# Kernel optimization log

Measured on AMD Instinct MI355X. Metric: run time of the kernel, lower is better.

## Reference

```python
import jax, jax.numpy as jnp
import numpy as np


def setup_inputs() -> dict:
    key = jax.random.key(0)
    kx, kw = jax.random.split(key)
    B, C, H, W, K = 16, 256, 128, 128, 7
    x = jax.random.normal(kx, (B, C, H, W), dtype=jnp.float32)
    # module initializes w with uniform(-0.1, 0.1)
    w = jax.random.uniform(kw, (C, K, K), dtype=jnp.float32, minval=-0.1, maxval=0.1)
    return {"x": x, "w": w}


def reference(x, w):
    # PolarConv2D forward intent: unfold(2,K,S).unfold(3,K,S) then per-channel
    # contraction of each (K,K) patch with w[c] -> depthwise convolution.
    # out[b,c,i,j] = sum_{k1,k2} x[b,c,i*S+k1, j*S+k2] * w[c,k1,k2]
    # Implemented as a grouped conv (feature_group_count=C) so the K*K-times
    # redundant unfolded tensor is never materialized.
    C = w.shape[0]
    kern = w[:, None, :, :]  # OIHW with I=1 (depthwise)
    out = jax.lax.conv_general_dilated(
        x, kern,
        window_strides=(1, 1),
        padding="VALID",
        dimension_numbers=("NCHW", "OIHW", "NCHW"),
        feature_group_count=C,
    )
    return out  # (B, C, H-K+1, W-K+1)
```

## Files before the change

### kernel.cpp

```cpp
#include <hip/hip_runtime.h>


#define BATCH 16
#define CHAN  256
#define H_IN  128
#define W_IN  128
#define KS    7
#define H_OUT 122
#define W_OUT 122

typedef float v2f __attribute__((ext_vector_type(2)));

__device__ __forceinline__ float sgpr_bcast(float v) {
    return __int_as_float(__builtin_amdgcn_readfirstlane(__float_as_int(v)));
}

__global__ __launch_bounds__(256)
void dwconv7x7_kernel(const float* __restrict__ x,
                      const float* __restrict__ w,
                      float* __restrict__ out) {
    const int lane = threadIdx.x & 63;
    const int img  = blockIdx.x;
    const int q    = threadIdx.x >> 6;
    const int ch   = img & (CHAN - 1);

    int c = 2 * lane;
    if (lane >= 32) c -= 6;
    const int r0 = 30 * q;

    const float* __restrict__ wp = w + ch * (KS * KS);
    float wr[KS * KS];
    #pragma unroll
    for (int i = 0; i < KS * KS; ++i) wr[i] = sgpr_bcast(wp[i]);

    const float* __restrict__ xq =
        x + (size_t)img * (H_IN * W_IN) + (size_t)r0 * W_IN + c;
    float* __restrict__ oq =
        out + (size_t)img * (H_OUT * W_OUT) + (size_t)r0 * W_OUT + c;

    float acc[KS][2] = {};
    float f[8];

    #define LOADW() do {                                                   \
        const v2f a0 = *reinterpret_cast<const v2f*>(xq);                  \
        const v2f a1 = *reinterpret_cast<const v2f*>(xq + 2);              \
        const v2f a2 = *reinterpret_cast<const v2f*>(xq + 4);              \
        const v2f a3 = *reinterpret_cast<const v2f*>(xq + 6);              \
        f[0] = a0.x; f[1] = a0.y; f[2] = a1.x; f[3] = a1.y;                \
        f[4] = a2.x; f[5] = a2.y; f[6] = a3.x; f[7] = a3.y; } while (0)

    #define ACCUM(SLOT, KY) do {                                           \
        _Pragma("unroll")                                                  \
        for (int kx = 0; kx < 7; ++kx) {                                   \
            const float wv = wr[(KY) * 7 + kx];                            \
            acc[(SLOT)][0] = fmaf(f[kx],     wv, acc[(SLOT)][0]);          \
            acc[(SLOT)][1] = fmaf(f[kx + 1], wv, acc[(SLOT)][1]);          \
        } } while (0)

    #define MAINSTEP(U) do {                                               \
        LOADW();                                                           \
        _Pragma("unroll")                                                  \
        for (int ky = 0; ky < KS; ++ky)                                    \
            ACCUM((6 + (U) - ky + 7) % KS, ky);                            \
        v2f v; v.x = acc[(U)][0]; v.y = acc[(U)][1];                       \
        __builtin_nontemporal_store(v, reinterpret_cast<v2f*>(oq));        \
        acc[(U)][0] = 0.f; acc[(U)][1] = 0.f;                              \
        xq += W_IN; oq += W_OUT; } while (0)

    #pragma unroll
    for (int s = 0; s < 6; ++s) {
        LOADW();
        #pragma unroll
        for (int ky = 0; ky <= s; ++ky)
            ACCUM((s - ky) % KS, ky);
        xq += W_IN;
    }

    for (int sb = 0; sb < 4; ++sb) {
        #pragma unroll
        for (int u = 0; u < 7; ++u) {
            MAINSTEP(u);
        }
    }

    #pragma unroll
    for (int t = 0; t < 4; ++t) {
        MAINSTEP(t);
    }

    #undef LOADW
    #undef ACCUM
    #undef MAINSTEP
}

extern "C" void kernel_launch(void* const* d_in, const int* in_sizes, int n_in,
                              void* d_out, int out_size, void* d_ws, size_t ws_size,
                              hipStream_t stream) {
    const float* x = (const float*)d_in[0];
    const float* w = (const float*)d_in[1];
    float* out = (float*)d_out;

    dim3 grid(BATCH * CHAN, 1, 1);
    dim3 block(256, 1, 1);
    dwconv7x7_kernel<<<grid, block, 0, stream>>>(x, w, out);
}
```

Baseline: 95.44 us.

## Stage input rows into LDS via async global_load_lds with multi-buffered pipeline

Instead of each lane loading overlapping 8-float windows straight from global memory, each wave asynchronously copies pairs of input rows into a 4-slot LDS ring buffer using global_load_lds. Manual vmcnt waits keep several row stages in flight while FMAs run. The accumulation is also reorganised into packed v2f FMAs over an 8-slot rotating accumulator. The hand-tuned waitcnt values and the LDS aliasing across stages carry correctness risk, and the removed compiler-visible memory dependencies could hide races because there is no barrier between LDS writes and reads.

```diff
diff --git a/kernel.cpp b/kernel.cpp
--- a/kernel.cpp
+++ b/kernel.cpp
@@ -1,4 +1,5 @@
 #include <hip/hip_runtime.h>
+#include <stdint.h>
 
 
 #define BATCH 16
@@ -19,9 +20,11 @@
 void dwconv7x7_kernel(const float* __restrict__ x,
                       const float* __restrict__ w,
                       float* __restrict__ out) {
+    __shared__ float lds[4][4][256];
+
     const int lane = threadIdx.x & 63;
+    const int q    = threadIdx.x >> 6;
     const int img  = blockIdx.x;
-    const int q    = threadIdx.x >> 6;
     const int ch   = img & (CHAN - 1);
 
     int c = 2 * lane;
@@ -33,64 +36,114 @@
     #pragma unroll
     for (int i = 0; i < KS * KS; ++i) wr[i] = sgpr_bcast(wp[i]);
 
-    const float* __restrict__ xq =
-        x + (size_t)img * (H_IN * W_IN) + (size_t)r0 * W_IN + c;
-    float* __restrict__ oq =
+    const float* xstage =
+        x + (size_t)img * (H_IN * W_IN) + (size_t)r0 * W_IN + lane * 4;
+    float* oq =
         out + (size_t)img * (H_OUT * W_OUT) + (size_t)r0 * W_OUT + c;
 
-    float acc[KS][2] = {};
-    float f[8];
+    v2f acc[8];
+    #pragma unroll
+    for (int i = 0; i < 8; ++i) { acc[i].x = 0.f; acc[i].y = 0.f; }
 
-    #define LOADW() do {                                                   \
-        const v2f a0 = *reinterpret_cast<const v2f*>(xq);                  \
-        const v2f a1 = *reinterpret_cast<const v2f*>(xq + 2);              \
-        const v2f a2 = *reinterpret_cast<const v2f*>(xq + 4);              \
-        const v2f a3 = *reinterpret_cast<const v2f*>(xq + 6);              \
-        f[0] = a0.x; f[1] = a0.y; f[2] = a1.x; f[3] = a1.y;                \
-        f[4] = a2.x; f[5] = a2.y; f[6] = a3.x; f[7] = a3.y; } while (0)
+    #define STAGE(SLOT) do {                                               \
+        asm volatile("" ::: "memory");                                     \
+        __builtin_amdgcn_global_load_lds(                                  \
+            (const __attribute__((address_space(1))) void*)xstage,         \
+            (__attribute__((address_space(3))) void*)&lds[q][SLOT][0],     \
+            16, 0, 0);                                                     \
+        xstage += 2 * W_IN; } while (0)
 
-    #define ACCUM(SLOT, KY) do {                                           \
+    #define WAITV(N) asm volatile("s_waitcnt vmcnt(" #N ")" ::: "memory")
+
+    #define ROWD(SM8, LSLOT, HALF, KYLO, KYHI) do {                        \
+        const float* rl = &lds[q][LSLOT][(HALF) * 128];                    \
+        const v2f p0 = *(const v2f*)(rl + c);                              \
+        const v2f p1 = *(const v2f*)(rl + c + 2);                          \
+        const v2f p2 = *(const v2f*)(rl + c + 4);                          \
+        const v2f p3 = *(const v2f*)(rl + c + 6);                          \
+        v2f s0, s1, s2;                                                    \
+        s0.x = p0.y; s0.y = p1.x;                                          \
+        s1.x = p1.y; s1.y = p2.x;                                          \
+        s2.x = p2.y; s2.y = p3.x;                                          \
+        const v2f srcv[7] = {p0, s0, p1, s1, p2, s2, p3};                  \
         _Pragma("unroll")                                                  \
-        for (int kx = 0; kx < 7; ++kx) {                                   \
-            const float wv = wr[(KY) * 7 + kx];                            \
-            acc[(SLOT)][0] = fmaf(f[kx],     wv, acc[(SLOT)][0]);          \
-            acc[(SLOT)][1] = fmaf(f[kx + 1], wv, acc[(SLOT)][1]);          \
+        for (int ky = (KYLO); ky <= (KYHI); ++ky) {                        \
+            _Pragma("unroll")                                              \
+            for (int kx = 0; kx < 7; ++kx) {                               \
+                const float wv = wr[ky * 7 + kx];                          \
+                v2f wpair; wpair.x = wv; wpair.y = wv;                     \
+                acc[((SM8) - ky + 8) & 7] = __builtin_elementwise_fma(     \
+                    srcv[kx], wpair, acc[((SM8) - ky + 8) & 7]);           \
+            }                                                              \
         } } while (0)
 
-    #define MAINSTEP(U) do {                                               \
-        LOADW();                                                           \
-        _Pragma("unroll")                                                  \
-        for (int ky = 0; ky < KS; ++ky)                                    \
-            ACCUM((6 + (U) - ky + 7) % KS, ky);                            \
-        v2f v; v.x = acc[(U)][0]; v.y = acc[(U)][1];                       \
-        __builtin_nontemporal_store(v, reinterpret_cast<v2f*>(oq));        \
-        acc[(U)][0] = 0.f; acc[(U)][1] = 0.f;                              \
-        xq += W_IN; oq += W_OUT; } while (0)
+    #define ST(OSLOT) do {                                                 \
+        __builtin_nontemporal_store(acc[OSLOT], (v2f*)oq);                 \
+        acc[OSLOT].x = 0.f; acc[OSLOT].y = 0.f;                           \
+        oq += W_OUT; } while (0)
 
-    #pragma unroll
-    for (int s = 0; s < 6; ++s) {
-        LOADW();
-        #pragma unroll
-        for (int ky = 0; ky <= s; ++ky)
-            ACCUM((s - ky) % KS, ky);
-        xq += W_IN;
+    #define STSKIP(OSLOT) do {                                             \
+        if (q == 0) __builtin_nontemporal_store(acc[OSLOT], (v2f*)oq);     \
+        acc[OSLOT].x = 0.f; acc[OSLOT].y = 0.f;                           \
+        oq += W_OUT; } while (0)
+
+    STAGE(0); STAGE(1); STAGE(2);
+
+    STAGE(3); WAITV(3);
+    ROWD(0, 0, 0, 0, 0);
+    ROWD(1, 0, 1, 0, 1);
+    STAGE(0); WAITV(3);
+    ROWD(2, 1, 0, 0, 2);
+    ROWD(3, 1, 1, 0, 3);
+    STAGE(1); WAITV(3);
+    ROWD(4, 2, 0, 0, 4);
+    ROWD(5, 2, 1, 0, 5);
+    STAGE(2); WAITV(3);
+    ROWD(6, 3, 0, 0, 6); STSKIP(0);
+    ROWD(7, 3, 1, 0, 6); STSKIP(1);
+    STAGE(3); WAITV(3);
+    ROWD(0, 0, 0, 0, 6); ST(2);
+    ROWD(1, 0, 1, 0, 6); ST(3);
+    STAGE(0); WAITV(5);
+    ROWD(2, 1, 0, 0, 6); ST(4);
+    ROWD(3, 1, 1, 0, 6); ST(5);
+    STAGE(1); WAITV(7);
+    ROWD(4, 2, 0, 0, 6); ST(6);
+    ROWD(5, 2, 1, 0, 6); ST(7);
+
+    for (int rep = 0; rep < 2; ++rep) {
+        STAGE(2); WAITV(9);
+        ROWD(6, 3, 0, 0, 6); ST(0);
+        ROWD(7, 3, 1, 0, 6); ST(1);
+        STAGE(3); WAITV(9);
+        ROWD(0, 0, 0, 0, 6); ST(2);
+        ROWD(1, 0, 1, 0, 6); ST(3);
+        STAGE(0); WAITV(9);
+        ROWD(2, 1, 0, 0, 6); ST(4);
+        ROWD(3, 1, 1, 0, 6); ST(5);
+        STAGE(1); WAITV(9);
+        ROWD(4, 2, 0, 0, 6); ST(6);
+        ROWD(5, 2, 1, 0, 6); ST(7);
     }
 
-    for (int sb = 0; sb < 4; ++sb) {
-        #pragma unroll
-        for (int u = 0; u < 7; ++u) {
-            MAINSTEP(u);
-        }
-    }
+    STAGE(2); WAITV(9);
+    ROWD(6, 3, 0, 0, 6); ST(0);
+    ROWD(7, 3, 1, 0, 6); ST(1);
+    WAITV(8);
+    ROWD(0, 0, 0, 1, 6); ST(2);
+    ROWD(1, 0, 1, 2, 6); ST(3);
+    WAITV(7);
+    ROWD(2, 1, 0, 3, 6); ST(4);
+    ROWD(3, 1, 1, 4, 6); ST(5);
+    WAITV(6);
+    ROWD(4, 2, 0, 5, 6); ST(6);
+    ROWD(5, 2, 1, 6, 6); ST(7);
 
-    #pragma unroll
-    for (int t = 0; t < 4; ++t) {
-        MAINSTEP(t);
-    }
-
-    #undef LOADW
-    #undef ACCUM
-    #undef MAINSTEP
+    #undef STAGE
+    #undef WAITV
+    #undef ROWD
+    #undef ST
+    #undef STSKIP
 }
 
 extern "C" void kernel_launch(void* const* d_in, const int* in_sizes, int n_in,
```

Measured after the change: 93.98 us (median of 2 runs). No clear change (-1.5%).
